# Optimization experiments

Measured on AMD Instinct MI355X. Metric: run time of the kernel, lower is better.

The kernel has to match this reference:

```python
import jax, jax.numpy as jnp
import numpy as np

H = 64          # hidden_feats
NODE_IN = 128
EDGE_IN = 16
N_NODES = 40000
N_EDGES = 80000
N_GRAPHS = 256
READOUT = 1024
N_MP = 3        # num_step_message_passing
N_S2S = 3       # num_step_set2set


def setup_inputs() -> dict:
    key = jax.random.key(0)
    ks = jax.random.split(key, 12)
    s = 0.05
    return {
        "node_feats": jax.random.normal(ks[0], (N_NODES, NODE_IN), jnp.float32),
        "edge_feats": jax.random.normal(ks[1], (N_EDGES, EDGE_IN), jnp.float32),
        "edge_src": jax.random.randint(ks[2], (N_EDGES,), 0, N_NODES, dtype=jnp.int32),
        "edge_dst": jax.random.randint(ks[3], (N_EDGES,), 0, N_NODES, dtype=jnp.int32),
        # evenly partition nodes into graphs (sorted, every graph non-empty)
        "node_graph_ids": (jnp.arange(N_NODES) * N_GRAPHS // N_NODES).astype(jnp.int32),
        # project_node_feats: Linear(node_in, H)
        "W_proj": jax.random.normal(ks[4], (H, NODE_IN), jnp.float32) * s,
        "b_proj": jnp.zeros((H,), jnp.float32),
        # edge network: Linear(edge_in, H*H)
        "W_edge": jax.random.normal(ks[5], (H * H, EDGE_IN), jnp.float32) * s,
        "b_edge": jnp.zeros((H * H,), jnp.float32),
        # NNConv bias
        "b_conv": jnp.zeros((H,), jnp.float32),
        # GRU(H, H), torch gate order r|z|n
        "gru_W_ih": jax.random.normal(ks[6], (3 * H, H), jnp.float32) * s,
        "gru_W_hh": jax.random.normal(ks[7], (3 * H, H), jnp.float32) * s,
        "gru_b_ih": jnp.zeros((3 * H,), jnp.float32),
        "gru_b_hh": jnp.zeros((3 * H,), jnp.float32),
        # Set2Set LSTM(input=4H, hidden=2H), torch gate order i|f|g|o
        "lstm_W_ih": jax.random.normal(ks[8], (8 * H, 4 * H), jnp.float32) * s,
        "lstm_W_hh": jax.random.normal(ks[9], (8 * H, 2 * H), jnp.float32) * s,
        "lstm_b_ih": jnp.zeros((8 * H,), jnp.float32),
        "lstm_b_hh": jnp.zeros((8 * H,), jnp.float32),
        # sparsify: Linear(4H, READOUT) + PReLU (single param, init 0.25)
        "W_sp": jax.random.normal(ks[10], (READOUT, 4 * H), jnp.float32) * s,
        "b_sp": jnp.zeros((READOUT,), jnp.float32),
        "prelu_w": jnp.array(0.25, jnp.float32),
    }


def _forward(node_feats, edge_feats, edge_src, edge_dst, node_graph_ids,
             W_proj, b_proj, W_edge, b_edge, b_conv,
             gru_W_ih, gru_W_hh, gru_b_ih, gru_b_hh,
             lstm_W_ih, lstm_W_hh, lstm_b_ih, lstm_b_hh,
             W_sp, b_sp, prelu_w):
    N = node_feats.shape[0]
    x0 = jax.nn.relu(node_feats @ W_proj.T + b_proj)            # (N, H)
    # edge-conditioned weights (computed once; torch recomputes identically per step)
    We = (edge_feats @ W_edge.T + b_edge).reshape(-1, H, H)     # (E, H, H)
    x, hid = x0, x0                                             # GRU h0 = projected node feats
    for _ in range(N_MP):
        # NNConv: gather src feats, per-edge matmul, scatter-sum to dst
        msg = jnp.einsum('eh,eho->eo', x[edge_src], We)         # (E, H)
        agg = jax.ops.segment_sum(msg, edge_dst, num_segments=N) + b_conv
        a = jax.nn.relu(agg)
        # GRUCell (seq_len=1)
        gi = a @ gru_W_ih.T + gru_b_ih
        gh = hid @ gru_W_hh.T + gru_b_hh
        i_r, i_z, i_n = jnp.split(gi, 3, axis=-1)
        h_r, h_z, h_n = jnp.split(gh, 3, axis=-1)
        r = jax.nn.sigmoid(i_r + h_r)
        z = jax.nn.sigmoid(i_z + h_z)
        n = jnp.tanh(i_n + r * h_n)
        hid = (1.0 - z) * n + z * hid
        x = hid
    feat = jnp.concatenate([x0, x], axis=1)                     # (N, 2H)
    D = 2 * H
    B = N_GRAPHS
    # Set2Set pooling
    q_star = jnp.zeros((B, 2 * D), feat.dtype)
    h_l = jnp.zeros((B, D), feat.dtype)
    c_l = jnp.zeros((B, D), feat.dtype)
    for _ in range(N_S2S):
        gates = q_star @ lstm_W_ih.T + lstm_b_ih + h_l @ lstm_W_hh.T + lstm_b_hh
        i_g, f_g, g_g, o_g = jnp.split(gates, 4, axis=-1)
        c_l = jax.nn.sigmoid(f_g) * c_l + jax.nn.sigmoid(i_g) * jnp.tanh(g_g)
        h_l = jax.nn.sigmoid(o_g) * jnp.tanh(c_l)
        q = h_l                                                 # (B, D)
        e = jnp.sum(feat * q[node_graph_ids], axis=-1)          # (N,)
        # segment softmax (every graph is non-empty by construction)
        e_max = jax.ops.segment_max(e, node_graph_ids, num_segments=B)
        ex = jnp.exp(e - e_max[node_graph_ids])
        denom = jax.ops.segment_sum(ex, node_graph_ids, num_segments=B)
        alpha = ex / denom[node_graph_ids]
        r_b = jax.ops.segment_sum(alpha[:, None] * feat, node_graph_ids, num_segments=B)
        q_star = jnp.concatenate([q, r_b], axis=-1)             # (B, 2D)
    out = q_star @ W_sp.T + b_sp                                # (B, READOUT)
    return jnp.where(out >= 0, out, prelu_w * out)              # PReLU


def reference(node_feats, edge_feats, edge_src, edge_dst, node_graph_ids,
              W_proj, b_proj, W_edge, b_edge, b_conv,
              gru_W_ih, gru_W_hh, gru_b_ih, gru_b_hh,
              lstm_W_ih, lstm_W_hh, lstm_b_ih, lstm_b_hh,
              W_sp, b_sp, prelu_w):
    return _forward(node_feats, edge_feats, edge_src, edge_dst, node_graph_ids,
                    W_proj, b_proj, W_edge, b_edge, b_conv,
                    gru_W_ih, gru_W_hh, gru_b_ih, gru_b_hh,
                    lstm_W_ih, lstm_W_hh, lstm_b_ih, lstm_b_hh,
                    W_sp, b_sp, prelu_w)
```

## Files before the change

### kernel.cpp

```cpp
#include <hip/hip_runtime.h>
#include <math.h>

#define H 64
#define NODE_IN 128
#define EDGE_IN 16
#define N_NODES 40000
#define N_EDGES 80000
#define N_GRAPHS 256
#define READOUT 1024
#define D2 128
#define QS 256

typedef unsigned short u16;
typedef __attribute__((ext_vector_type(8))) short bf16x8;
typedef __attribute__((ext_vector_type(4))) float f32x4;
#define MFMA16(a,b,c) __builtin_amdgcn_mfma_f32_16x16x32_bf16(a,b,c,0,0,0)

__device__ u16 d_xhi[N_NODES*H];
__device__ u16 d_xlo[N_NODES*H];
__device__ u16 d_we3T_hi[64*1088];
__device__ u16 d_bcT_hi[256*128];
__device__ float d_wspT[256*1024];

__device__ __forceinline__ float sigmoidf_(float x){ return 1.0f/(1.0f + expf(-x)); }

__device__ __forceinline__ u16 bf_hi(float x){
  union { float f; unsigned u; } c; c.f = x;
  unsigned r = (c.u + 0x7FFFu + ((c.u >> 16) & 1u)) >> 16;
  return (u16)r;
}
__device__ __forceinline__ float bf_f(u16 h){
  union { unsigned u; float f; } c; c.u = ((unsigned)h) << 16; return c.f;
}
__device__ __forceinline__ u16 bf_lo(float x, u16 hi){ return bf_hi(x - bf_f(hi)); }

__device__ __forceinline__ int swz(int row, int kq){
  return (row*128 + kq*16) ^ ((row & 7) << 4);
}

__device__ __forceinline__ bf16x8 rne8(const float* Z){
  union { bf16x8 v; u16 u[8]; } hh;
  #pragma unroll
  for (int k = 0; k < 8; ++k) hh.u[k] = bf_hi(Z[k]);
  return hh.v;
}

__global__ __launch_bounds__(256) void pack_we3T(
    const float* __restrict__ We, const float* __restrict__ be){
  int i = blockIdx.x*256 + threadIdx.x;
  int o = i / 1088, c = i % 1088;
  float v;
  if (c < 1024){
    int hh = c >> 4, k = c & 15;
    v = We[(size_t)(hh*64 + o)*EDGE_IN + k];
  } else {
    v = be[(size_t)(c - 1024)*64 + o];
  }
  d_we3T_hi[i] = bf_hi(v);
}

__global__ __launch_bounds__(256) void pack_bcT(
    const float* __restrict__ Wih, const float* __restrict__ Whh){
  int i = blockIdx.x*256 + threadIdx.x;
  int k = i >> 8, c = i & 255;
  float v;
  if (c < 128){
    v = (k < 64) ? Wih[(size_t)c*H + k] : Whh[(size_t)c*H + (k-64)];
  } else if (c < 192){
    int d = c - 128;
    v = (k < 64) ? Wih[(size_t)(128+d)*H + k] : 0.f;
  } else {
    int d = c - 192;
    v = (k < 64) ? 0.f : Whh[(size_t)(128+d)*H + (k-64)];
  }
  d_bcT_hi[c*128 + k] = bf_hi(v);
}

__global__ __launch_bounds__(256) void pack_wspT(const float* __restrict__ Wsp){
  int i = blockIdx.x*256 + threadIdx.x;
  int j = i >> 8, k = i & 255;
  d_wspT[(size_t)k*1024 + j] = Wsp[i];
}

__global__ __launch_bounds__(256) void zero_buf(float4* __restrict__ p, int n4){
  int i = blockIdx.x*256 + threadIdx.x;
  int stride = gridDim.x*256;
  for (; i < n4; i += stride) p[i] = make_float4(0.f,0.f,0.f,0.f);
}

__global__ __launch_bounds__(256) void proj_mm(
    const float* __restrict__ nf, const float* __restrict__ Wp,
    const float* __restrict__ bp, float* __restrict__ x0, float* __restrict__ h){
  __shared__ float A_s[NODE_IN][64];
  __shared__ float B_s[NODE_IN][64];
  int t = threadIdx.x;
  int nb = blockIdx.x * 64;
  #pragma unroll
  for (int p = 0; p < 8; ++p){
    int idx = p*256 + t;
    int n = idx >> 5, k4 = idx & 31;
    float4 v = ((const float4*)(nf + (size_t)(nb+n)*NODE_IN))[k4];
    int base = (((n>>2) ^ (k4 & 15)) << 2) + (n & 3);
    A_s[k4*4+0][base]=v.x; A_s[k4*4+1][base]=v.y;
    A_s[k4*4+2][base]=v.z; A_s[k4*4+3][base]=v.w;
  }
  #pragma unroll
  for (int p = 0; p < 8; ++p){
    int idx = p*256 + t;
    int c = idx & 63, k4 = idx >> 6;
    float4 v = ((const float4*)(Wp + (size_t)c*NODE_IN))[k4];
    B_s[k4*4+0][c]=v.x; B_s[k4*4+1][c]=v.y; B_s[k4*4+2][c]=v.z; B_s[k4*4+3][c]=v.w;
  }
  __syncthreads();
  int eg = t & 15, cg = t >> 4;
  float acc[4][4] = {};
  #pragma unroll 4
  for (int k = 0; k < NODE_IN; ++k){
    int s = (k >> 2) & 15;
    float4 a = *(const float4*)&A_s[k][(eg ^ s) << 2];
    float4 b = *(const float4*)&B_s[k][cg*4];
    float av[4] = {a.x,a.y,a.z,a.w};
    float bv[4] = {b.x,b.y,b.z,b.w};
    #pragma unroll
    for (int j = 0; j < 4; ++j)
      #pragma unroll
      for (int c = 0; c < 4; ++c) acc[j][c] += av[j]*bv[c];
  }
  float4 bb = ((const float4*)bp)[cg];
  float bv[4] = {bb.x,bb.y,bb.z,bb.w};
  #pragma unroll
  for (int j = 0; j < 4; ++j){
    int n = nb + eg*4 + j;
    float o[4];
    #pragma unroll
    for (int c = 0; c < 4; ++c) o[c] = fmaxf(acc[j][c]+bv[c], 0.f);
    *(float4*)(x0 + (size_t)n*H + cg*4) = make_float4(o[0],o[1],o[2],o[3]);
    *(float4*)(h  + (size_t)n*H + cg*4) = make_float4(o[0],o[1],o[2],o[3]);
    u16 hs[4], ls[4];
    #pragma unroll
    for (int c = 0; c < 4; ++c){ hs[c] = bf_hi(o[c]); ls[c] = bf_lo(o[c], hs[c]); }
    *(ushort4*)&d_xhi[(size_t)n*H + cg*4] = make_ushort4(hs[0],hs[1],hs[2],hs[3]);
    *(ushort4*)&d_xlo[(size_t)n*H + cg*4] = make_ushort4(ls[0],ls[1],ls[2],ls[3]);
  }
}

__global__ __launch_bounds__(256) void edge_mfma(
    const float* __restrict__ xf, const float* __restrict__ ef,
    const int* __restrict__ src, const int* __restrict__ dst,
    float* __restrict__ agg){
  __shared__ __align__(16) char smem[16384];
  __shared__ __align__(16) float x_s[64][68];
  __shared__ int src_s[64], dst_s[64];
  float* msg_s = (float*)x_s;

  int t = threadIdx.x;
  int w = t >> 6, lane = t & 63;
  int m = lane & 15, kq = lane >> 4;
  int ebase = blockIdx.x * 64;
  int e0 = t >> 2, j4 = t & 3;
  if (t < 64){ src_s[t] = src[ebase + t]; dst_s[t] = dst[ebase + t]; }
  {
    const u16* gh = d_we3T_hi + (size_t)e0*1088 + j4*16;
    int b0 = swz(e0, 2*j4), b1 = swz(e0, 2*j4+1);
    *(bf16x8*)(smem + b0) = *(const bf16x8*)gh;
    *(bf16x8*)(smem + b1) = *(const bf16x8*)(gh+8);
  }
  __syncthreads();
  {
    const float4* px = (const float4*)(xf + (size_t)src_s[e0]*H + j4*16);
    float4 v0=px[0], v1=px[1], v2=px[2], v3=px[3];
    float* xr = &x_s[e0][j4*16];
    *(float4*)xr      = v0;
    *(float4*)(xr+4)  = v1;
    *(float4*)(xr+8)  = v2;
    *(float4*)(xr+12) = v3;
  }
  int e = w*16 + m;
  float ef8[8];
  {
    const float4* p = (const float4*)(ef + (size_t)(ebase+e)*EDGE_IN + (kq&1)*8);
    float4 a = p[0], b = p[1];
    ef8[0]=a.x; ef8[1]=a.y; ef8[2]=a.z; ef8[3]=a.w;
    ef8[4]=b.x; ef8[5]=b.y; ef8[6]=b.z; ef8[7]=b.w;
  }
  __syncthreads();

  int hsel = kq >> 1;
  f32x4 acc[4];
  #pragma unroll
  for (int i = 0; i < 4; ++i) acc[i] = (f32x4){0.f,0.f,0.f,0.f};

  #pragma unroll 2
  for (int ci = 0; ci < 16; ++ci){
    bf16x8 pbh0, pbh1;
    {
      const u16* gh = d_we3T_hi + (size_t)e0*1088 + (ci+1)*64 + j4*16;
      pbh0 = *(const bf16x8*)gh; pbh1 = *(const bf16x8*)(gh+8);
    }
    float x0v = x_s[e][ci*4 + hsel];
    float x1v = x_s[e][ci*4 + 2 + hsel];
    float Z0[8], Z1[8];
    #pragma unroll
    for (int j = 0; j < 8; ++j){ Z0[j] = x0v*ef8[j]; Z1[j] = x1v*ef8[j]; }
    bf16x8 a0 = rne8(Z0), a1 = rne8(Z1);
    {
      char* BhC = smem + (ci & 1)*8192;
      #pragma unroll
      for (int nt = 0; nt < 4; ++nt){
        int rb = nt*16 + m;
        int c0 = swz(rb, kq), c1 = c0 ^ 64;
        bf16x8 bh0 = *(const bf16x8*)(BhC + c0);
        bf16x8 bh1 = *(const bf16x8*)(BhC + c1);
        acc[nt] = MFMA16(a0, bh0, acc[nt]);
        acc[nt] = MFMA16(a1, bh1, acc[nt]);
      }
    }
    {
      char* BhN = smem + ((ci+1) & 1)*8192;
      int b0 = swz(e0, 2*j4), b1 = swz(e0, 2*j4+1);
      *(bf16x8*)(BhN + b0) = pbh0;
      *(bf16x8*)(BhN + b1) = pbh1;
    }
    __syncthreads();
  }
  {
    float xb[16];
    {
      const float4* q0 = (const float4*)&x_s[e][kq*8];
      const float4* q1 = (const float4*)&x_s[e][32 + kq*8];
      float4 a=q0[0], b=q0[1], c=q1[0], d=q1[1];
      xb[0]=a.x; xb[1]=a.y; xb[2]=a.z; xb[3]=a.w;
      xb[4]=b.x; xb[5]=b.y; xb[6]=b.z; xb[7]=b.w;
      xb[8]=c.x; xb[9]=c.y; xb[10]=c.z; xb[11]=c.w;
      xb[12]=d.x; xb[13]=d.y; xb[14]=d.z; xb[15]=d.w;
    }
    bf16x8 a0 = rne8(xb), a1 = rne8(xb + 8);
    char* BhC = smem;
    #pragma unroll
    for (int nt = 0; nt < 4; ++nt){
      int rb = nt*16 + m;
      int c0 = swz(rb, kq), c1 = c0 ^ 64;
      bf16x8 bh0 = *(const bf16x8*)(BhC + c0);
      bf16x8 bh1 = *(const bf16x8*)(BhC + c1);
      acc[nt] = MFMA16(a0, bh0, acc[nt]);
      acc[nt] = MFMA16(a1, bh1, acc[nt]);
    }
  }
  __syncthreads();
  #pragma unroll
  for (int nt = 0; nt < 4; ++nt){
    int o = nt*16 + m;
    #pragma unroll
    for (int r = 0; r < 4; ++r){
      int ee = w*16 + kq*4 + r;
      msg_s[ee*64 + (o ^ ((ee & 7) << 2))] = acc[nt][r];
    }
  }
  __syncthreads();
  #pragma unroll
  for (int r = 0; r < 16; ++r){
    int ee = w*16 + r;
    atomicAdd(&agg[(size_t)dst_s[ee]*H + lane],
              msg_s[ee*64 + (lane ^ ((ee & 7) << 2))]);
  }
}

__global__ __launch_bounds__(256) void gru_mm_mfma(
    float* __restrict__ agg, const float* __restrict__ bconv,
    float* __restrict__ h, const float* __restrict__ gbih,
    const float* __restrict__ gbhh){
  __shared__ u16 Ah[64][40], Al[64][40];
  __shared__ u16 Bh[256][40];
  __shared__ float bih_s[192], bhh_s[192];
  int t = threadIdx.x;
  int w = t >> 6, lane = t & 63;
  int nb = blockIdx.x * 64;
  if (t < 192){ bih_s[t] = gbih[t]; bhh_s[t] = gbhh[t]; }
  int m = lane & 15, kj = (lane >> 4) * 8;
  f32x4 acc[16];
  #pragma unroll
  for (int i = 0; i < 16; ++i) acc[i] = (f32x4){0.f,0.f,0.f,0.f};
  bf16x8 pbh[4];
  #pragma unroll
  for (int qq = 0; qq < 4; ++qq)
    pbh[qq] = *(const bf16x8*)&d_bcT_hi[t*128 + qq*8];
  for (int kc = 0; kc < 4; ++kc){
    __syncthreads();
    {
      int n = t >> 2, q = t & 3;
      if (kc < 2){
        float* sp = agg + (size_t)(nb+n)*H + kc*32 + q*8;
        float4 v0 = *(const float4*)sp;
        float4 v1 = *(const float4*)(sp + 4);
        float4 b0 = *(const float4*)&bconv[kc*32 + q*8];
        float4 b1 = *(const float4*)&bconv[kc*32 + q*8 + 4];
        *(float4*)sp       = make_float4(0.f,0.f,0.f,0.f);
        *(float4*)(sp + 4) = make_float4(0.f,0.f,0.f,0.f);
        float vals[8] = { fmaxf(v0.x+b0.x,0.f), fmaxf(v0.y+b0.y,0.f),
                          fmaxf(v0.z+b0.z,0.f), fmaxf(v0.w+b0.w,0.f),
                          fmaxf(v1.x+b1.x,0.f), fmaxf(v1.y+b1.y,0.f),
                          fmaxf(v1.z+b1.z,0.f), fmaxf(v1.w+b1.w,0.f) };
        union { bf16x8 v; u16 u[8]; } ph, pl;
        #pragma unroll
        for (int j = 0; j < 8; ++j){
          u16 hi = bf_hi(vals[j]);
          ph.u[j] = hi; pl.u[j] = bf_lo(vals[j], hi);
        }
        *(bf16x8*)&Ah[n][q*8] = ph.v;
        *(bf16x8*)&Al[n][q*8] = pl.v;
      } else {
        int gofs = (nb+n)*H + (kc-2)*32 + q*8;
        *(bf16x8*)&Ah[n][q*8] = *(const bf16x8*)&d_xhi[gofs];
        *(bf16x8*)&Al[n][q*8] = *(const bf16x8*)&d_xlo[gofs];
      }
    }
    #pragma unroll
    for (int qq = 0; qq < 4; ++qq)
      *(bf16x8*)&Bh[t][qq*8] = pbh[qq];
    if (kc < 3){
      #pragma unroll
      for (int qq = 0; qq < 4; ++qq)
        pbh[qq] = *(const bf16x8*)&d_bcT_hi[t*128 + (kc+1)*32 + qq*8];
    }
    __syncthreads();
    bf16x8 ah = *(const bf16x8*)&Ah[w*16 + m][kj];
    bf16x8 al = *(const bf16x8*)&Al[w*16 + m][kj];
    #pragma unroll
    for (int nt = 0; nt < 16; ++nt){
      bf16x8 bh = *(const bf16x8*)&Bh[nt*16 + m][kj];
      acc[nt] = MFMA16(ah, bh, acc[nt]);
      acc[nt] = MFMA16(al, bh, acc[nt]);
    }
  }
  int q4 = lane >> 4, col0 = lane & 15;
  #pragma unroll
  for (int r = 0; r < 4; ++r){
    int node = nb + w*16 + q4*4 + r;
    #pragma unroll
    for (int j = 0; j < 4; ++j){
      int d = col0 + 16*j;
      float rg = sigmoidf_(acc[j][r]   + bih_s[d]      + bhh_s[d]);
      float z  = sigmoidf_(acc[4+j][r] + bih_s[64+d]   + bhh_s[64+d]);
      float nn = tanhf(acc[8+j][r] + bih_s[128+d] + rg*(acc[12+j][r] + bhh_s[128+d]));
      size_t off = (size_t)node*H + d;
      float hv = h[off];
      float hn = (1.f - z)*nn + z*hv;
      h[off] = hn;
      u16 hb = bf_hi(hn);
      d_xhi[off] = hb;
      d_xlo[off] = bf_lo(hn, hb);
    }
  }
}

__global__ __launch_bounds__(256) void build_bl2(
    const float* __restrict__ Wih, const float* __restrict__ Whh,
    float* __restrict__ Bl2){
  int i = blockIdx.x*256 + threadIdx.x;
  int k = i >> 9, c = i & 511;
  int d = c >> 2, gate = c & 3;
  int row = gate*128 + d;
  float v = (k < 256) ? Wih[(size_t)row*QS + k] : Whh[(size_t)row*D2 + (k-256)];
  Bl2[i] = v;
}

__global__ __launch_bounds__(512) void s2s_kernel(
    const float* __restrict__ x0, const float* __restrict__ h,
    const float* __restrict__ Bl2, const float* __restrict__ lbih,
    const float* __restrict__ lbhh, float* __restrict__ hl,
    float* __restrict__ cl, float* __restrict__ qstar){
  __shared__ float A_s[384];
  __shared__ float part4[4][128][4];
  __shared__ float q_s[D2];
  __shared__ float alpha_s[160];
  __shared__ float wred[8];
  __shared__ float part[8][D2];
  int g = blockIdx.x, t = threadIdx.x;
  int lane = t & 63, w = t >> 6;
  if (t < 384){
    A_s[t] = (t < 256) ? qstar[(size_t)g*QS + t] : hl[(size_t)g*D2 + (t - 256)];
  }
  __syncthreads();
  {
    int d = t & 127, ks = t >> 7;
    const float* bp = Bl2 + 4*d;
    float ai = 0.f, af = 0.f, ag = 0.f, ao = 0.f;
    #pragma unroll 8
    for (int kk = 0; kk < 96; ++kk){
      int k = ks*96 + kk;
      float a = A_s[k];
      float4 b = *(const float4*)(bp + (size_t)k*512);
      ai += a*b.x; af += a*b.y; ag += a*b.z; ao += a*b.w;
    }
    *(float4*)&part4[ks][d][0] = make_float4(ai, af, ag, ao);
  }
  __syncthreads();
  if (t < D2){
    float4 p0 = *(const float4*)&part4[0][t][0];
    float4 p1 = *(const float4*)&part4[1][t][0];
    float4 p2 = *(const float4*)&part4[2][t][0];
    float4 p3 = *(const float4*)&part4[3][t][0];
    float iv = p0.x+p1.x+p2.x+p3.x + lbih[t]       + lbhh[t];
    float fv = p0.y+p1.y+p2.y+p3.y + lbih[128 + t] + lbhh[128 + t];
    float gv = p0.z+p1.z+p2.z+p3.z + lbih[256 + t] + lbhh[256 + t];
    float ov = p0.w+p1.w+p2.w+p3.w + lbih[384 + t] + lbhh[384 + t];
    float c = sigmoidf_(fv)*cl[(size_t)g*D2 + t] + sigmoidf_(iv)*tanhf(gv);
    float hn = sigmoidf_(ov)*tanhf(c);
    cl[(size_t)g*D2 + t] = c;
    hl[(size_t)g*D2 + t] = hn;
    q_s[t] = hn;
  }
  __syncthreads();
  int n0 = (g*N_NODES + N_GRAPHS - 1)/N_GRAPHS;
  int n1 = ((g+1)*N_NODES + N_GRAPHS - 1)/N_GRAPHS;
  int cnt = n1 - n0;
  float e = -1e30f;
  if (t < cnt){
    int n = n0 + t;
    const float4* xr = (const float4*)(x0 + (size_t)n*H);
    const float4* hr = (const float4*)(h  + (size_t)n*H);
    const float4* q1 = (const float4*)q_s;
    const float4* q2 = (const float4*)(q_s + H);
    float s = 0.0f;
    #pragma unroll
    for (int k4 = 0; k4 < 16; ++k4){
      float4 a = xr[k4], b = q1[k4];
      s += a.x*b.x + a.y*b.y + a.z*b.z + a.w*b.w;
    }
    #pragma unroll
    for (int k4 = 0; k4 < 16; ++k4){
      float4 a = hr[k4], b = q2[k4];
      s += a.x*b.x + a.y*b.y + a.z*b.z + a.w*b.w;
    }
    e = s;
  }
  float mx = e;
  #pragma unroll
  for (int off = 32; off >= 1; off >>= 1) mx = fmaxf(mx, __shfl_xor(mx, off));
  if (lane == 0) wred[w] = mx;
  __syncthreads();
  float gm = wred[0];
  #pragma unroll
  for (int i = 1; i < 8; ++i) gm = fmaxf(gm, wred[i]);
  __syncthreads();
  float ex = (t < cnt) ? expf(e - gm) : 0.0f;
  float sm = ex;
  #pragma unroll
  for (int off = 32; off >= 1; off >>= 1) sm += __shfl_xor(sm, off);
  if (lane == 0) wred[w] = sm;
  __syncthreads();
  float denom = wred[0]+wred[1]+wred[2]+wred[3]+wred[4]+wred[5]+wred[6]+wred[7];
  if (t < cnt) alpha_s[t] = ex / denom;
  __syncthreads();
  float acc0 = 0.f, acc1 = 0.f;
  for (int i = w; i < cnt; i += 8){
    float a = alpha_s[i];
    acc0 += a * x0[(size_t)(n0+i)*H + lane];
    acc1 += a * h [(size_t)(n0+i)*H + lane];
  }
  part[w][lane]      = acc0;
  part[w][64 + lane] = acc1;
  __syncthreads();
  if (t < D2){
    float v = 0.f;
    #pragma unroll
    for (int i = 0; i < 8; ++i) v += part[i][t];
    qstar[(size_t)g*QS + t]      = q_s[t];
    qstar[(size_t)g*QS + D2 + t] = v;
  }
}

__global__ __launch_bounds__(256) void out_kernel(
    const float* __restrict__ qstar, const float* __restrict__ bsp,
    const float* __restrict__ prelu, float* __restrict__ out){
  __shared__ float q_s[QS];
  int g = blockIdx.x >> 1, half = blockIdx.x & 1;
  int t = threadIdx.x;
  q_s[t] = qstar[(size_t)g*QS + t];
  __syncthreads();
  int j0 = half*512 + t;
  float acc0 = bsp[j0], acc1 = bsp[j0 + 256];
  const float* wp = d_wspT + j0;
  #pragma unroll 4
  for (int k = 0; k < QS; ++k){
    float q = q_s[k];
    acc0 += q * wp[(size_t)k*1024];
    acc1 += q * wp[(size_t)k*1024 + 256];
  }
  float pw = prelu[0];
  out[(size_t)g*READOUT + j0]       = (acc0 >= 0.0f) ? acc0 : pw*acc0;
  out[(size_t)g*READOUT + j0 + 256] = (acc1 >= 0.0f) ? acc1 : pw*acc1;
}

extern "C" void kernel_launch(void* const* d_in, const int* in_sizes, int n_in,
                              void* d_out, int out_size, void* d_ws, size_t ws_size,
                              hipStream_t stream) {
  const float* node_feats = (const float*)d_in[0];
  const float* edge_feats = (const float*)d_in[1];
  const int*   esrc       = (const int*)d_in[2];
  const int*   edst       = (const int*)d_in[3];
  const float* Wproj = (const float*)d_in[5];
  const float* bproj = (const float*)d_in[6];
  const float* Wedge = (const float*)d_in[7];
  const float* bedge = (const float*)d_in[8];
  const float* bconv = (const float*)d_in[9];
  const float* gWih  = (const float*)d_in[10];
  const float* gWhh  = (const float*)d_in[11];
  const float* gbih  = (const float*)d_in[12];
  const float* gbhh  = (const float*)d_in[13];
  const float* lWih  = (const float*)d_in[14];
  const float* lWhh  = (const float*)d_in[15];
  const float* lbih  = (const float*)d_in[16];
  const float* lbhh  = (const float*)d_in[17];
  const float* Wsp   = (const float*)d_in[18];
  const float* bsp   = (const float*)d_in[19];
  const float* prelu = (const float*)d_in[20];

  float* ws    = (float*)d_ws;
  float* x0    = ws;
  float* h     = ws + 2560000;
  float* agg   = ws + 5120000;
  float* qstar = ws + 7680000;
  float* hl    = qstar + 65536;
  float* cl    = hl + 32768;
  float* Bl2   = agg;

  hipMemsetAsync(qstar, 0, (65536 + 32768 + 32768)*sizeof(float), stream);

  pack_we3T<<<272, 256, 0, stream>>>(Wedge, bedge);
  pack_bcT<<<128, 256, 0, stream>>>(gWih, gWhh);
  pack_wspT<<<1024, 256, 0, stream>>>(Wsp);

  proj_mm<<<N_NODES/64, 256, 0, stream>>>(node_feats, Wproj, bproj, x0, h);

  for (int s = 0; s < 3; ++s){
    if (s == 0)
      zero_buf<<<2048, 256, 0, stream>>>((float4*)agg, N_NODES*H/4);
    edge_mfma<<<N_EDGES/64, 256, 0, stream>>>(h, edge_feats, esrc, edst, agg);
    gru_mm_mfma<<<N_NODES/64, 256, 0, stream>>>(agg, bconv, h, gbih, gbhh);
  }

  build_bl2<<<768, 256, 0, stream>>>(lWih, lWhh, Bl2);

  for (int s = 0; s < 3; ++s){
    s2s_kernel<<<N_GRAPHS, 512, 0, stream>>>(x0, h, Bl2, lbih, lbhh, hl, cl, qstar);
  }

  out_kernel<<<2*N_GRAPHS, 256, 0, stream>>>(qstar, bsp, prelu, (float*)d_out);
}
```

Measured before the change: 312.8 us.

## Pre-pack weights in MFMA fragment order and load B operands directly from global

```diff
diff --git a/kernel.cpp b/kernel.cpp
--- a/kernel.cpp
+++ b/kernel.cpp
@@ -18,8 +18,8 @@
 
 __device__ u16 d_xhi[N_NODES*H];
 __device__ u16 d_xlo[N_NODES*H];
-__device__ u16 d_we3T_hi[64*1088];
-__device__ u16 d_bcT_hi[256*128];
+__device__ u16 d_weF[17*4*2*64*8];
+__device__ u16 d_bcF[4*16*64*8];
 __device__ float d_wspT[256*1024];
 
 __device__ __forceinline__ float sigmoidf_(float x){ return 1.0f/(1.0f + expf(-x)); }
@@ -34,10 +34,6 @@
 }
 __device__ __forceinline__ u16 bf_lo(float x, u16 hi){ return bf_hi(x - bf_f(hi)); }
 
-__device__ __forceinline__ int swz(int row, int kq){
-  return (row*128 + kq*16) ^ ((row & 7) << 4);
-}
-
 __device__ __forceinline__ bf16x8 rne8(const float* Z){
   union { bf16x8 v; u16 u[8]; } hh;
   #pragma unroll
@@ -45,35 +41,35 @@
   return hh.v;
 }
 
-__global__ __launch_bounds__(256) void pack_we3T(
+__global__ __launch_bounds__(256) void pack_weF(
     const float* __restrict__ We, const float* __restrict__ be){
   int i = blockIdx.x*256 + threadIdx.x;
-  int o = i / 1088, c = i % 1088;
-  float v;
-  if (c < 1024){
-    int hh = c >> 4, k = c & 15;
-    v = We[(size_t)(hh*64 + o)*EDGE_IN + k];
-  } else {
-    v = be[(size_t)(c - 1024)*64 + o];
-  }
-  d_we3T_hi[i] = bf_hi(v);
-}
-
-__global__ __launch_bounds__(256) void pack_bcT(
+  int j = i & 7, lane = (i >> 3) & 63, half = (i >> 9) & 1;
+  int nt = (i >> 10) & 3, ci = i >> 12;
+  int o = nt*16 + (lane & 15);
+  int c = ci*64 + half*32 + (lane >> 4)*8 + j;
+  float v = (c < 1024) ? We[(size_t)((c >> 4)*64 + o)*EDGE_IN + (c & 15)]
+                       : be[(size_t)(c - 1024)*64 + o];
+  d_weF[i] = bf_hi(v);
+}
+
+__global__ __launch_bounds__(256) void pack_bcF(
     const float* __restrict__ Wih, const float* __restrict__ Whh){
   int i = blockIdx.x*256 + threadIdx.x;
-  int k = i >> 8, c = i & 255;
+  int j = i & 7, lane = (i >> 3) & 63, nt = (i >> 9) & 15, kc = i >> 13;
+  int cr = nt*16 + (lane & 15);
+  int k  = kc*32 + (lane >> 4)*8 + j;
   float v;
-  if (c < 128){
-    v = (k < 64) ? Wih[(size_t)c*H + k] : Whh[(size_t)c*H + (k-64)];
-  } else if (c < 192){
-    int d = c - 128;
+  if (cr < 128){
+    v = (k < 64) ? Wih[(size_t)cr*H + k] : Whh[(size_t)cr*H + (k-64)];
+  } else if (cr < 192){
+    int d = cr - 128;
     v = (k < 64) ? Wih[(size_t)(128+d)*H + k] : 0.f;
   } else {
-    int d = c - 192;
+    int d = cr - 192;
     v = (k < 64) ? 0.f : Whh[(size_t)(128+d)*H + (k-64)];
   }
-  d_bcT_hi[c*128 + k] = bf_hi(v);
+  d_bcF[i] = bf_hi(v);
 }
 
 __global__ __launch_bounds__(256) void pack_wspT(const float* __restrict__ Wsp){
@@ -148,26 +144,15 @@
     const float* __restrict__ xf, const float* __restrict__ ef,
     const int* __restrict__ src, const int* __restrict__ dst,
     float* __restrict__ agg){
-  __shared__ __align__(16) char smem[16384];
   __shared__ __align__(16) float x_s[64][68];
-  __shared__ int src_s[64], dst_s[64];
-  float* msg_s = (float*)x_s;
-
   int t = threadIdx.x;
   int w = t >> 6, lane = t & 63;
   int m = lane & 15, kq = lane >> 4;
   int ebase = blockIdx.x * 64;
   int e0 = t >> 2, j4 = t & 3;
-  if (t < 64){ src_s[t] = src[ebase + t]; dst_s[t] = dst[ebase + t]; }
   {
-    const u16* gh = d_we3T_hi + (size_t)e0*1088 + j4*16;
-    int b0 = swz(e0, 2*j4), b1 = swz(e0, 2*j4+1);
-    *(bf16x8*)(smem + b0) = *(const bf16x8*)gh;
-    *(bf16x8*)(smem + b1) = *(const bf16x8*)(gh+8);
-  }
-  __syncthreads();
-  {
-    const float4* px = (const float4*)(xf + (size_t)src_s[e0]*H + j4*16);
+    int s0 = src[ebase + e0];
+    const float4* px = (const float4*)(xf + (size_t)s0*H + j4*16);
     float4 v0=px[0], v1=px[1], v2=px[2], v3=px[3];
     float* xr = &x_s[e0][j4*16];
     *(float4*)xr      = v0;
@@ -183,45 +168,27 @@
     ef8[0]=a.x; ef8[1]=a.y; ef8[2]=a.z; ef8[3]=a.w;
     ef8[4]=b.x; ef8[5]=b.y; ef8[6]=b.z; ef8[7]=b.w;
   }
-  __syncthreads();
-
   int hsel = kq >> 1;
+  const bf16x8* wF = (const bf16x8*)d_weF + lane;
   f32x4 acc[4];
   #pragma unroll
   for (int i = 0; i < 4; ++i) acc[i] = (f32x4){0.f,0.f,0.f,0.f};
 
   #pragma unroll 2
   for (int ci = 0; ci < 16; ++ci){
-    bf16x8 pbh0, pbh1;
-    {
-      const u16* gh = d_we3T_hi + (size_t)e0*1088 + (ci+1)*64 + j4*16;
-      pbh0 = *(const bf16x8*)gh; pbh1 = *(const bf16x8*)(gh+8);
-    }
     float x0v = x_s[e][ci*4 + hsel];
     float x1v = x_s[e][ci*4 + 2 + hsel];
     float Z0[8], Z1[8];
     #pragma unroll
     for (int j = 0; j < 8; ++j){ Z0[j] = x0v*ef8[j]; Z1[j] = x1v*ef8[j]; }
     bf16x8 a0 = rne8(Z0), a1 = rne8(Z1);
-    {
-      char* BhC = smem + (ci & 1)*8192;
-      #pragma unroll
-      for (int nt = 0; nt < 4; ++nt){
-        int rb = nt*16 + m;
-        int c0 = swz(rb, kq), c1 = c0 ^ 64;
-        bf16x8 bh0 = *(const bf16x8*)(BhC + c0);
-        bf16x8 bh1 = *(const bf16x8*)(BhC + c1);
-        acc[nt] = MFMA16(a0, bh0, acc[nt]);
-        acc[nt] = MFMA16(a1, bh1, acc[nt]);
-      }
-    }
-    {
-      char* BhN = smem + ((ci+1) & 1)*8192;
-      int b0 = swz(e0, 2*j4), b1 = swz(e0, 2*j4+1);
-      *(bf16x8*)(BhN + b0) = pbh0;
-      *(bf16x8*)(BhN + b1) = pbh1;
-    }
-    __syncthreads();
+    #pragma unroll
+    for (int nt = 0; nt < 4; ++nt){
+      bf16x8 b0 = wF[(size_t)((ci*4+nt)*2 + 0)*64];
+      bf16x8 b1 = wF[(size_t)((ci*4+nt)*2 + 1)*64];
+      acc[nt] = MFMA16(a0, b0, acc[nt]);
+      acc[nt] = MFMA16(a1, b1, acc[nt]);
+    }
   }
   {
     float xb[16];
@@ -235,33 +202,30 @@
       xb[12]=d.x; xb[13]=d.y; xb[14]=d.z; xb[15]=d.w;
     }
     bf16x8 a0 = rne8(xb), a1 = rne8(xb + 8);
-    char* BhC = smem;
     #pragma unroll
     for (int nt = 0; nt < 4; ++nt){
-      int rb = nt*16 + m;
-      int c0 = swz(rb, kq), c1 = c0 ^ 64;
-      bf16x8 bh0 = *(const bf16x8*)(BhC + c0);
-      bf16x8 bh1 = *(const bf16x8*)(BhC + c1);
-      acc[nt] = MFMA16(a0, bh0, acc[nt]);
-      acc[nt] = MFMA16(a1, bh1, acc[nt]);
-    }
-  }
-  __syncthreads();
+      bf16x8 b0 = wF[(size_t)((64+nt)*2 + 0)*64];
+      bf16x8 b1 = wF[(size_t)((64+nt)*2 + 1)*64];
+      acc[nt] = MFMA16(a0, b0, acc[nt]);
+      acc[nt] = MFMA16(a1, b1, acc[nt]);
+    }
+  }
+  float* msg_s = (float*)x_s;
   #pragma unroll
   for (int nt = 0; nt < 4; ++nt){
     int o = nt*16 + m;
     #pragma unroll
     for (int r = 0; r < 4; ++r){
       int ee = w*16 + kq*4 + r;
-      msg_s[ee*64 + (o ^ ((ee & 7) << 2))] = acc[nt][r];
-    }
-  }
-  __syncthreads();
+      msg_s[ee*68 + (o ^ ((ee & 7) << 2))] = acc[nt][r];
+    }
+  }
   #pragma unroll
   for (int r = 0; r < 16; ++r){
     int ee = w*16 + r;
-    atomicAdd(&agg[(size_t)dst_s[ee]*H + lane],
-              msg_s[ee*64 + (lane ^ ((ee & 7) << 2))]);
+    int dn = dst[ebase + ee];
+    atomicAdd(&agg[(size_t)dn*H + lane],
+              msg_s[ee*68 + (lane ^ ((ee & 7) << 2))]);
   }
 }
 
@@ -270,22 +234,17 @@
     float* __restrict__ h, const float* __restrict__ gbih,
     const float* __restrict__ gbhh){
   __shared__ u16 Ah[64][40], Al[64][40];
-  __shared__ u16 Bh[256][40];
   __shared__ float bih_s[192], bhh_s[192];
   int t = threadIdx.x;
   int w = t >> 6, lane = t & 63;
   int nb = blockIdx.x * 64;
   if (t < 192){ bih_s[t] = gbih[t]; bhh_s[t] = gbhh[t]; }
   int m = lane & 15, kj = (lane >> 4) * 8;
+  const bf16x8* bF = (const bf16x8*)d_bcF + lane;
   f32x4 acc[16];
   #pragma unroll
   for (int i = 0; i < 16; ++i) acc[i] = (f32x4){0.f,0.f,0.f,0.f};
-  bf16x8 pbh[4];
-  #pragma unroll
-  for (int qq = 0; qq < 4; ++qq)
-    pbh[qq] = *(const bf16x8*)&d_bcT_hi[t*128 + qq*8];
   for (int kc = 0; kc < 4; ++kc){
-    __syncthreads();
     {
       int n = t >> 2, q = t & 3;
       if (kc < 2){
@@ -314,24 +273,16 @@
         *(bf16x8*)&Al[n][q*8] = *(const bf16x8*)&d_xlo[gofs];
       }
     }
-    #pragma unroll
-    for (int qq = 0; qq < 4; ++qq)
-      *(bf16x8*)&Bh[t][qq*8] = pbh[qq];
-    if (kc < 3){
-      #pragma unroll
-      for (int qq = 0; qq < 4; ++qq)
-        pbh[qq] = *(const bf16x8*)&d_bcT_hi[t*128 + (kc+1)*32 + qq*8];
-    }
-    __syncthreads();
     bf16x8 ah = *(const bf16x8*)&Ah[w*16 + m][kj];
     bf16x8 al = *(const bf16x8*)&Al[w*16 + m][kj];
     #pragma unroll
     for (int nt = 0; nt < 16; ++nt){
-      bf16x8 bh = *(const bf16x8*)&Bh[nt*16 + m][kj];
+      bf16x8 bh = bF[(size_t)(kc*16 + nt)*64];
       acc[nt] = MFMA16(ah, bh, acc[nt]);
       acc[nt] = MFMA16(al, bh, acc[nt]);
     }
   }
+  __syncthreads();
   int q4 = lane >> 4, col0 = lane & 15;
   #pragma unroll
   for (int r = 0; r < 4; ++r){
@@ -527,8 +478,8 @@
 
   hipMemsetAsync(qstar, 0, (65536 + 32768 + 32768)*sizeof(float), stream);
 
-  pack_we3T<<<272, 256, 0, stream>>>(Wedge, bedge);
-  pack_bcT<<<128, 256, 0, stream>>>(gWih, gWhh);
+  pack_weF<<<272, 256, 0, stream>>>(Wedge, bedge);
+  pack_bcF<<<128, 256, 0, stream>>>(gWih, gWhh);
   pack_wspT<<<1024, 256, 0, stream>>>(Wsp);
 
   proj_mm<<<N_NODES/64, 256, 0, stream>>>(node_feats, Wproj, bproj, x0, h);
```

Result: no change. 313.1 us (median of 2 runs) (+0.1%).
